# Kernel tuning notes

Hardware: AMD Instinct MI355X
Metric: run time of the kernel (lower is better)

The kernel has to match this reference:

```python
import jax, jax.numpy as jnp
import numpy as np
from jax import lax

EPS = 1e-5
KH = KW = 3
K = KH * KW


def conv3x3(x, w, b=None):
    # x: [B,Cin,H,W], w: [Cout,Cin,3,3], padding=1, stride=1
    y = lax.conv_general_dilated(x, w, (1, 1), [(1, 1), (1, 1)],
                                 dimension_numbers=("NCHW", "OIHW", "NCHW"))
    if b is not None:
        y = y + b[None, :, None, None]
    return y


def deform_conv2d(x, offset, mask, weight):
    # torchvision-style deform_conv2d v2: kernel 3x3, stride 1, pad 1, dilation 1,
    # groups=1, offset_groups=1. offset: [B,2K,H,W] (dy,dx per tap), mask: [B,K,H,W].
    B, C, H, W = x.shape
    off = offset.reshape(B, K, 2, H, W)
    kidx = jnp.arange(K)
    kdy = (kidx // KW - 1).astype(x.dtype)[None, :, None, None]  # [1,K,1,1]
    kdx = (kidx % KW - 1).astype(x.dtype)[None, :, None, None]
    yy = jnp.arange(H, dtype=x.dtype)[None, None, :, None]
    xx = jnp.arange(W, dtype=x.dtype)[None, None, None, :]
    py = yy + kdy + off[:, :, 0]  # [B,K,H,W] sampling rows
    px = xx + kdx + off[:, :, 1]  # [B,K,H,W] sampling cols

    y0 = jnp.floor(py).astype(jnp.int32)
    x0 = jnp.floor(px).astype(jnp.int32)
    wy = py - y0.astype(x.dtype)
    wx = px - x0.astype(x.dtype)

    def gather_b(xb, yc, xc):
        # xb: [C,H,W]; yc, xc: [K,H,W] -> [C,K,H,W], zeros outside image
        valid = (yc >= 0) & (yc < H) & (xc >= 0) & (xc < W)
        v = xb[:, jnp.clip(yc, 0, H - 1), jnp.clip(xc, 0, W - 1)]
        return v * valid[None].astype(xb.dtype)

    gather = jax.vmap(gather_b, in_axes=(0, 0, 0))  # over batch

    w00 = ((1 - wy) * (1 - wx))[:, None]  # [B,1,K,H,W]
    w01 = ((1 - wy) * wx)[:, None]
    w10 = (wy * (1 - wx))[:, None]
    w11 = (wy * wx)[:, None]

    sampled = (gather(x, y0, x0) * w00 + gather(x, y0, x0 + 1) * w01 +
               gather(x, y0 + 1, x0) * w10 + gather(x, y0 + 1, x0 + 1) * w11)
    sampled = sampled * mask[:, None]  # [B,C,K,H,W]
    wk = weight.reshape(weight.shape[0], weight.shape[1], K)
    return jnp.einsum("bckhw,ock->bohw", sampled, wk)


def reference(f1_feat, f3_feat, offset_w, offset_b, main_w, gamma, beta):
    concat = jnp.concatenate([f1_feat, f3_feat], axis=1)
    om = conv3x3(concat, offset_w, offset_b)  # [B,27,H,W]
    offset = om[:, :18]
    mask = jax.nn.sigmoid(om[:, 18:])
    aligned = deform_conv2d(f1_feat, offset, mask, main_w)
    # BatchNorm2d, training mode (batch statistics, biased variance)
    mean = aligned.mean(axis=(0, 2, 3))
    var = aligned.var(axis=(0, 2, 3))
    xn = (aligned - mean[None, :, None, None]) * lax.rsqrt(var + EPS)[None, :, None, None]
    return xn * gamma[None, :, None, None] + beta[None, :, None, None]


def setup_inputs() -> dict:
    key = jax.random.key(0)
    ks = jax.random.split(key, 5)
    B, C, H, W = 4, 64, 128, 128
    f1 = jax.random.normal(ks[0], (B, C, H, W), jnp.float32)
    f3 = jax.random.normal(ks[1], (B, C, H, W), jnp.float32)
    # small offset-conv init so predicted offsets stay in-image (like trained nets)
    offset_w = jax.random.normal(ks[2], (27, 2 * C, 3, 3), jnp.float32) * 0.01
    offset_b = jnp.zeros((27,), jnp.float32)
    main_w = jax.random.normal(ks[3], (C, C, 3, 3), jnp.float32) * (1.0 / np.sqrt(C * 9))
    gamma = jnp.ones((C,), jnp.float32)
    beta = jnp.zeros((C,), jnp.float32)
    return {"f1_feat": f1, "f3_feat": f3, "offset_w": offset_w,
            "offset_b": offset_b, "main_w": main_w, "gamma": gamma, "beta": beta}
```

## Files before the change

### kernel.cpp

```cpp
#include <hip/hip_runtime.h>
#include <math.h>

#define BB 4
#define CC 64
#define HH 128
#define WW 128
#define HWP 16384

typedef _Float16 h2 __attribute__((ext_vector_type(2)));
typedef _Float16 h4 __attribute__((ext_vector_type(4)));
typedef __fp16  p2 __attribute__((ext_vector_type(2)));
typedef float f32x4 __attribute__((ext_vector_type(4)));
union HU { unsigned u; h2 h; p2 p; };
union U2H { uint2 u; h4 h; };
static __device__ __forceinline__ h2 u2h(unsigned x){ HU v; v.u = x; return v.h; }
static __device__ __forceinline__ unsigned h2u(h2 x){ HU v; v.h = x; return v.u; }
static __device__ __forceinline__ unsigned pk2u(float a, float b){
    HU v; v.p = __builtin_amdgcn_cvt_pkrtz(a, b); return v.u;
}

__global__ __launch_bounds__(256) void kTm(
    const float* __restrict__ f1, const float* __restrict__ f3,
    const float* __restrict__ ow, const float* __restrict__ mw,
    unsigned* __restrict__ f13t, unsigned* __restrict__ wmf,
    unsigned* __restrict__ wof)
{
    __shared__ float lt[64*129];
    int t = threadIdx.x;
    if (blockIdx.x < 512) {
        int b = blockIdx.x >> 7, y = blockIdx.x & 127;
        unsigned* dst = f13t + ((size_t)((b << 14) + (y << 7)))*64;
        for (int half = 0; half < 2; ++half) {
            const float* src = (half == 0 ? f1 : f3) + (((size_t)b*64) << 14) + (y << 7);
#pragma unroll 4
            for (int i = 0; i < 32; ++i) {
                int idx = i*256 + t; int c = idx >> 7, x = idx & 127;
                lt[c*129 + x] = src[(c << 14) + x];
            }
            __syncthreads();
#pragma unroll 4
            for (int i = 0; i < 16; ++i) {
                int idx = i*256 + t; int x = idx >> 5, cp = idx & 31;
                dst[x*64 + half*32 + cp] = pk2u(lt[(2*cp)*129 + x], lt[(2*cp+1)*129 + x]);
            }
            __syncthreads();
        }
        return;
    }
    int i = (blockIdx.x - 512)*256 + t;
    if (i < 18432) {
        int j   = i & 1;
        int t2  = i >> 1;
        int kb  = t2 % 36;
        int rl  = t2 / 36;
        int l   = rl & 63;
        int r   = rl >> 6;
        int row = l & 15, ksel = l >> 4;
        int och = r*16 + row;
        int P   = kb*8 + ksel*2 + j;
        int kt  = P >> 5;
        int cp  = P & 31;
        float lo = mw[och*576 + (2*cp    )*9 + kt];
        float hi = mw[och*576 + (2*cp + 1)*9 + kt];
        wmf[i] = pk2u(lo, hi);
    } else if (i < 36864) {
        int idx = i - 18432;
        int j   = idx & 1;
        int t2  = idx >> 1;
        int kb  = t2 % 72;
        int rl  = t2 / 72;
        int l   = rl & 63;
        int mt  = rl >> 6;
        int row = l & 15, ksel = l >> 4;
        int och = mt*16 + row;
        int P   = kb*8 + ksel*2 + j;
        int kt  = P >> 6;
        int cp  = P & 63;
        unsigned v = 0;
        if (och < 27) {
            float lo = ow[(och*128 + 2*cp    )*9 + kt];
            float hi = ow[(och*128 + 2*cp + 1)*9 + kt];
            v = pk2u(lo, hi);
        }
        wof[idx] = v;
    }
}

__global__ __launch_bounds__(256) void k1_offset_conv(
    const unsigned* __restrict__ f13t, const unsigned* __restrict__ wof,
    const float* __restrict__ ob, float* __restrict__ om)
{
    __shared__ unsigned tile[34*68];

    int blk0 = blockIdx.x;
    int blk  = ((blk0 & 7) << 8) | (blk0 >> 3);
    int xq = blk & 3;
    int y  = (blk >> 2) & 127;
    int b  = blk >> 9;

    int tid  = threadIdx.x;
    int lane = tid & 63;
    int wv   = tid >> 6;
    int mt   = wv >> 1;
    int pxt  = wv & 1;
    int row  = lane & 15;
    int ksel = lane >> 4;

    f32x4 acc = {0.f, 0.f, 0.f, 0.f};
    const unsigned* wbase = wof + (size_t)(mt*64 + lane)*144;

#pragma unroll 1
    for (int dy = 0; dy < 3; ++dy) {
        int yy = y + dy - 1;
        bool yok = (unsigned)yy < (unsigned)HH;
        __syncthreads();
        for (int i = tid; i < 544; i += 256) {
            int px34 = i >> 4, q = i & 15;
            int gxp = xq*32 - 1 + px34;
            uint4 v = make_uint4(0u, 0u, 0u, 0u);
            if (yok && (unsigned)gxp < (unsigned)WW)
                v = *(const uint4*)&f13t[(((size_t)(b*128 + yy))*128 + gxp)*64 + q*4];
            *(uint4*)&tile[px34*68 + q*4] = v;
        }
        __syncthreads();

#pragma unroll
        for (int hf = 0; hf < 2; ++hf) {
            uint4 wq[6];
#pragma unroll
            for (int m = 0; m < 6; ++m)
                wq[m] = *(const uint4*)&wbase[dy*48 + hf*24 + m*4];
#pragma unroll
            for (int kl = 0; kl < 12; ++kl) {
                int Pl  = (hf*12 + kl)*8 + ksel*2;
                int ktl = Pl >> 6;
                int cp  = Pl & 63;
                U2H wa;
                uint4 q = wq[kl >> 1];
                if (kl & 1) { wa.u.x = q.z; wa.u.y = q.w; }
                else        { wa.u.x = q.x; wa.u.y = q.y; }
                U2H bfr;
                bfr.u = *(const uint2*)&tile[(pxt*16 + row + ktl)*68 + cp];
                acc = __builtin_amdgcn_mfma_f32_16x16x16f16(wa.h, bfr.h, acc, 0, 0, 0);
            }
        }
    }

    int gx = xq*32 + pxt*16 + row;
#pragma unroll
    for (int rI = 0; rI < 4; ++rI) {
        int och = mt*16 + ksel*4 + rI;
        if (och < 27) {
            float v = acc[rI] + ob[och];
            if (och >= 18) v = 1.f / (1.f + __expf(-v));
            om[((b*27 + och) << 14) + (y << 7) + gx] = v;
        }
    }
}

__global__ __launch_bounds__(256) void k2_deform(
    const unsigned* __restrict__ f13t, const unsigned* __restrict__ wmf,
    const float* __restrict__ om, unsigned* __restrict__ alignedh,
    float* __restrict__ part)
{
    extern __shared__ unsigned lds[];
    unsigned* pl_a = lds;
    unsigned* pl_w = lds + 288;
    unsigned* sl   = lds + 864;

    int blk0 = blockIdx.x;
    int blk  = ((blk0 & 7) << 8) | (blk0 >> 3);
    int xq = blk & 3;
    int y  = (blk >> 2) & 127;
    int b  = blk >> 9;

    int tid  = threadIdx.x;
    int lane = tid & 63;
    int wv   = tid >> 6;
    int row  = lane & 15;
    int ksel = lane >> 4;
    int cg   = tid & 7;
    int grp  = tid >> 3;
    int pwb  = ((cg >> 2) << 4) | ((cg & 1) << 3) | (((cg >> 1) & 1) << 1);

    const float* omb = om + ((b*27) << 14) + (y << 7);
    const unsigned* ftb = f13t + (((size_t)b) << 20);

    for (int i = tid; i < 288; i += 256) {
        int k = i >> 5, lpx = i & 31;
        int gxp = xq*32 + lpx;
        float off0 = omb[((2*k)   << 14) + gxp];
        float off1 = omb[((2*k+1) << 14) + gxp];
        float mk   = omb[((18+k)  << 14) + gxp];

        float pyf = (float)y   + (float)(k/3) - 1.f + off0;
        float pxg = (float)gxp + (float)(k%3) - 1.f + off1;
        float fy = floorf(pyf), fx = floorf(pxg);
        int y0 = (int)fy, x0 = (int)fx;
        float wy = pyf - fy, wx = pxg - fx;
        float oy = 1.f - wy, ox = 1.f - wx;
        bool yv0 = (unsigned)y0     < (unsigned)HH;
        bool yv1 = (unsigned)(y0+1) < (unsigned)HH;
        bool xv0 = (unsigned)x0     < (unsigned)WW;
        bool xv1 = (unsigned)(x0+1) < (unsigned)WW;
        int y0c = min(max(y0, 0), 127);
        int x0c = min(max(x0, 0), 127);
        int dy = min(max(y0+1, 0), 127) - y0c;
        int dx = min(max(x0+1, 0), 127) - x0c;
        unsigned a = (unsigned)((y0c << 7) + x0c) | ((unsigned)dx << 14) | ((unsigned)dy << 15);
        float w00 = (yv0 && xv0) ? oy*ox*mk : 0.f;
        float w01 = (yv0 && xv1) ? oy*wx*mk : 0.f;
        float w10 = (yv1 && xv0) ? wy*ox*mk : 0.f;
        float w11 = (yv1 && xv1) ? wy*wx*mk : 0.f;
        pl_a[i] = a;
        pl_w[i*2]     = pk2u(w00, w01);
        pl_w[i*2 + 1] = pk2u(w10, w11);
    }
    __syncthreads();

    f32x4 acc0 = {0.f, 0.f, 0.f, 0.f};
    f32x4 acc1 = {0.f, 0.f, 0.f, 0.f};

    const unsigned* wbase = wmf + (wv*64 + lane)*72;

#pragma unroll 1
    for (int th = 0; th < 3; ++th) {
        uint4 wq[6];
#pragma unroll
        for (int m = 0; m < 6; ++m)
            wq[m] = *(const uint4*)&wbase[th*24 + m*4];

#pragma unroll
        for (int it = 0; it < 3; ++it) {
            int item = it*32 + grp;
            int ktl  = item >> 5;
            int px   = item & 31;
            int k    = th*3 + ktl;
            int pidx = k*32 + px;
            unsigned a = pl_a[pidx];
            uint2 wpk = *(const uint2*)&pl_w[pidx*2];
            int i00 = (int)(a & 0x3FFFu);
            int dx  = (int)((a >> 14) & 1u);
            int i10 = i00 + (((int)(a >> 15) & 1) << 7);
            h2 hw01 = u2h(wpk.x);
            h2 hw23 = u2h(wpk.y);
            h2 w00d = {hw01.x, hw01.x}, w01d = {hw01.y, hw01.y};
            h2 w10d = {hw23.x, hw23.x}, w11d = {hw23.y, hw23.y};

            uint4 t00 = *(const uint4*)&ftb[(size_t)(i00     )*64 + 4*cg];
            uint4 t01 = *(const uint4*)&ftb[(size_t)(i00 + dx)*64 + 4*cg];
            uint4 t10 = *(const uint4*)&ftb[(size_t)(i10     )*64 + 4*cg];
            uint4 t11 = *(const uint4*)&ftb[(size_t)(i10 + dx)*64 + 4*cg];

            h2 v0 = u2h(t00.x)*w00d + u2h(t01.x)*w01d + u2h(t10.x)*w10d + u2h(t11.x)*w11d;
            h2 v1 = u2h(t00.y)*w00d + u2h(t01.y)*w01d + u2h(t10.y)*w10d + u2h(t11.y)*w11d;
            h2 v2 = u2h(t00.z)*w00d + u2h(t01.z)*w01d + u2h(t10.z)*w10d + u2h(t11.z)*w11d;
            h2 v3 = u2h(t00.w)*w00d + u2h(t01.w)*w01d + u2h(t10.w)*w10d + u2h(t11.w)*w11d;

            int bs = px*100 + ktl*32 + pwb;
            *(uint2*)&sl[bs]     = make_uint2(h2u(v0), h2u(v1));
            *(uint2*)&sl[bs + 4] = make_uint2(h2u(v2), h2u(v3));
        }
        __syncthreads();

        const unsigned* b0p = &sl[(row     )*100 + ksel*4];
        const unsigned* b1p = &sl[(16+row  )*100 + ksel*4];
#pragma unroll
        for (int m = 0; m < 6; ++m) {
            uint4 bv0 = *(const uint4*)&b0p[m*16];
            uint4 bv1 = *(const uint4*)&b1p[m*16];
            U2H waA, waB, s0a, s0b, s1a, s1b;
            waA.u.x = wq[m].x; waA.u.y = wq[m].y;
            waB.u.x = wq[m].z; waB.u.y = wq[m].w;
            s0a.u.x = bv0.x; s0a.u.y = bv0.y;
            s0b.u.x = bv0.z; s0b.u.y = bv0.w;
            s1a.u.x = bv1.x; s1a.u.y = bv1.y;
            s1b.u.x = bv1.z; s1b.u.y = bv1.w;
            acc0 = __builtin_amdgcn_mfma_f32_16x16x16f16(waA.h, s0a.h, acc0, 0, 0, 0);
            acc0 = __builtin_amdgcn_mfma_f32_16x16x16f16(waB.h, s0b.h, acc0, 0, 0, 0);
            acc1 = __builtin_amdgcn_mfma_f32_16x16x16f16(waA.h, s1a.h, acc1, 0, 0, 0);
            acc1 = __builtin_amdgcn_mfma_f32_16x16x16f16(waB.h, s1b.h, acc1, 0, 0, 0);
        }
        __syncthreads();
    }

    float* sred = (float*)lds;
    int obase = ((b*CC) << 13) + (y << 6) + (xq << 4);
#pragma unroll
    for (int rI = 0; rI < 4; ++rI) {
        int och = wv*16 + ksel*4 + rI;
        float v0 = acc0[rI], v1 = acc1[rI];
        alignedh[obase + (och << 13) + row] = pk2u(v0, v1);
        float s  = v0 + v1;
        float sq = v0*v0 + v1*v1;
#pragma unroll
        for (int off = 1; off < 16; off <<= 1) {
            s  += __shfl_xor(s,  off, 64);
            sq += __shfl_xor(sq, off, 64);
        }
        if (row == 0) { sred[och] = s; sred[64 + och] = sq; }
    }
    __syncthreads();
    for (int i = tid; i < 128; i += 256)
        part[(size_t)blk*128 + i] = sred[i];
}

__global__ __launch_bounds__(256) void k3b_reduce(
    const float* __restrict__ part, float* __restrict__ stats)
{
    int i = blockIdx.x;
    int tid = threadIdx.x;
    float s = 0.f;
    for (int j = tid; j < 2048; j += 256) s += part[(size_t)j*128 + i];
    for (int off = 32; off > 0; off >>= 1) s += __shfl_down(s, off, 64);
    __shared__ float rs[4];
    int w = tid >> 6;
    if ((tid & 63) == 0) rs[w] = s;
    __syncthreads();
    if (tid == 0) stats[i] = rs[0] + rs[1] + rs[2] + rs[3];
}

__global__ __launch_bounds__(256) void k4_norm(
    const unsigned* __restrict__ alignedh, const float* __restrict__ stats,
    const float* __restrict__ gamma, const float* __restrict__ beta,
    float* __restrict__ out)
{
    const float invN = 1.f / 65536.f;
    int i4 = blockIdx.x*256 + threadIdx.x;
    int u  = i4 << 2;
    int c  = (u >> 13) & 63;
    int lx = u & 15;
    int xq = (u >> 4) & 3;
    int y  = (u >> 6) & 127;
    int bc = u >> 13;

    float mean = stats[c] * invN;
    float var  = stats[64 + c] * invN - mean*mean;
    float sc = gamma[c] * rsqrtf(var + 1e-5f);
    float sh = beta[c] - mean*sc;

    uint4 v = *(const uint4*)&alignedh[u];
    h2 p0 = u2h(v.x), p1 = u2h(v.y), p2 = u2h(v.z), p3 = u2h(v.w);
    float4 lo = make_float4((float)p0.x*sc + sh, (float)p1.x*sc + sh,
                            (float)p2.x*sc + sh, (float)p3.x*sc + sh);
    float4 hi = make_float4((float)p0.y*sc + sh, (float)p1.y*sc + sh,
                            (float)p2.y*sc + sh, (float)p3.y*sc + sh);
    int ob = (bc << 14) + (y << 7) + xq*32 + lx;
    *(float4*)&out[ob]      = lo;
    *(float4*)&out[ob + 16] = hi;
}

extern "C" void kernel_launch(void* const* d_in, const int* in_sizes, int n_in,
                              void* d_out, int out_size, void* d_ws, size_t ws_size,
                              hipStream_t stream)
{
    const float* f1    = (const float*)d_in[0];
    const float* f3    = (const float*)d_in[1];
    const float* ow    = (const float*)d_in[2];
    const float* ob    = (const float*)d_in[3];
    const float* mw    = (const float*)d_in[4];
    const float* gamma = (const float*)d_in[5];
    const float* beta  = (const float*)d_in[6];
    float* out = (float*)d_out;

    float* om     = (float*)d_ws;
    float* stats  = om + 4*27*HWP;
    unsigned* wmf = (unsigned*)(stats + 512);
    unsigned* wof = wmf + 18432;
    unsigned* f13t = wof + 18432;
    float* part   = (float*)(f13t + 4*HWP*64);
    unsigned* alignedh = (unsigned*)(part + 2048*128);

    const int lds2 = (864 + 32*100) * 4;
    (void)hipFuncSetAttribute((const void*)k2_deform,
        hipFuncAttributeMaxDynamicSharedMemorySize, lds2);

    hipLaunchKernelGGL(kTm, dim3(656), dim3(256), 0, stream,
                       f1, f3, ow, mw, f13t, wmf, wof);
    hipLaunchKernelGGL(k1_offset_conv, dim3(2048), dim3(256), 0, stream,
                       f13t, wof, ob, om);
    hipLaunchKernelGGL(k2_deform, dim3(2048), dim3(256), lds2, stream,
                       f13t, wmf, om, alignedh, part);
    hipLaunchKernelGGL(k3b_reduce, dim3(128), dim3(256), 0, stream, part, stats);
    hipLaunchKernelGGL(k4_norm, dim3(2048), dim3(256), 0, stream,
                       alignedh, stats, gamma, beta, out);
}
```

Before: 78.38 us.

## Compute two output rows per block in offset conv, reusing halo rows and weights

The offset-conv kernel now handles two output rows per block instead of one. It loads all four needed input rows into a larger dynamic LDS buffer with a single barrier, and each wave computes 32 pixels using two accumulators that share each weight fragment. This cuts redundant halo-row loads, weight fetches from global memory and barriers, and halves the grid to 1024 blocks. In exchange, LDS per block grows to about 37KB, which may lower occupancy, and the reduced grid leaves less parallelism.

```diff
diff --git a/kernel.cpp b/kernel.cpp
--- a/kernel.cpp
+++ b/kernel.cpp
@@ -90,40 +90,46 @@
     const unsigned* __restrict__ f13t, const unsigned* __restrict__ wof,
     const float* __restrict__ ob, float* __restrict__ om)
 {
-    __shared__ unsigned tile[34*68];
+    extern __shared__ unsigned tile[];
 
     int blk0 = blockIdx.x;
-    int blk  = ((blk0 & 7) << 8) | (blk0 >> 3);
+    int blk  = ((blk0 & 7) << 7) | (blk0 >> 3);
     int xq = blk & 3;
-    int y  = (blk >> 2) & 127;
-    int b  = blk >> 9;
+    int yp = (blk >> 2) & 63;
+    int b  = blk >> 8;
+    int y0r = yp << 1;
 
     int tid  = threadIdx.x;
     int lane = tid & 63;
     int wv   = tid >> 6;
     int mt   = wv >> 1;
-    int pxt  = wv & 1;
+    int ys   = wv & 1;
     int row  = lane & 15;
     int ksel = lane >> 4;
 
-    f32x4 acc = {0.f, 0.f, 0.f, 0.f};
-    const unsigned* wbase = wof + (size_t)(mt*64 + lane)*144;
-
 #pragma unroll 1
-    for (int dy = 0; dy < 3; ++dy) {
-        int yy = y + dy - 1;
+    for (int s = 0; s < 4; ++s) {
+        int yy = y0r + s - 1;
         bool yok = (unsigned)yy < (unsigned)HH;
-        __syncthreads();
+        unsigned* ts = tile + s*2312;
         for (int i = tid; i < 544; i += 256) {
             int px34 = i >> 4, q = i & 15;
             int gxp = xq*32 - 1 + px34;
             uint4 v = make_uint4(0u, 0u, 0u, 0u);
             if (yok && (unsigned)gxp < (unsigned)WW)
                 v = *(const uint4*)&f13t[(((size_t)(b*128 + yy))*128 + gxp)*64 + q*4];
-            *(uint4*)&tile[px34*68 + q*4] = v;
-        }
-        __syncthreads();
-
+            *(uint4*)&ts[px34*68 + q*4] = v;
+        }
+    }
+    __syncthreads();
+
+    f32x4 acc0 = {0.f, 0.f, 0.f, 0.f};
+    f32x4 acc1 = {0.f, 0.f, 0.f, 0.f};
+    const unsigned* wbase = wof + (size_t)(mt*64 + lane)*144;
+
+#pragma unroll 1
+    for (int dy = 0; dy < 3; ++dy) {
+        const unsigned* ts = tile + (ys + dy)*2312;
 #pragma unroll
         for (int hf = 0; hf < 2; ++hf) {
             uint4 wq[6];
@@ -139,21 +145,30 @@
                 uint4 q = wq[kl >> 1];
                 if (kl & 1) { wa.u.x = q.z; wa.u.y = q.w; }
                 else        { wa.u.x = q.x; wa.u.y = q.y; }
-                U2H bfr;
-                bfr.u = *(const uint2*)&tile[(pxt*16 + row + ktl)*68 + cp];
-                acc = __builtin_amdgcn_mfma_f32_16x16x16f16(wa.h, bfr.h, acc, 0, 0, 0);
+                U2H b0, b1;
+                b0.u = *(const uint2*)&ts[(row + ktl)*68 + cp];
+                b1.u = *(const uint2*)&ts[(16 + row + ktl)*68 + cp];
+                acc0 = __builtin_amdgcn_mfma_f32_16x16x16f16(wa.h, b0.h, acc0, 0, 0, 0);
+                acc1 = __builtin_amdgcn_mfma_f32_16x16x16f16(wa.h, b1.h, acc1, 0, 0, 0);
             }
         }
     }
 
-    int gx = xq*32 + pxt*16 + row;
+    int y  = y0r + ys;
+    int gx0 = xq*32 + row;
 #pragma unroll
     for (int rI = 0; rI < 4; ++rI) {
         int och = mt*16 + ksel*4 + rI;
         if (och < 27) {
-            float v = acc[rI] + ob[och];
-            if (och >= 18) v = 1.f / (1.f + __expf(-v));
-            om[((b*27 + och) << 14) + (y << 7) + gx] = v;
+            float v0 = acc0[rI] + ob[och];
+            float v1 = acc1[rI] + ob[och];
+            if (och >= 18) {
+                v0 = 1.f / (1.f + __expf(-v0));
+                v1 = 1.f / (1.f + __expf(-v1));
+            }
+            int base = ((b*27 + och) << 14) + (y << 7) + gx0;
+            om[base]      = v0;
+            om[base + 16] = v1;
         }
     }
 }
@@ -371,13 +386,16 @@
     float* part   = (float*)(f13t + 4*HWP*64);
     unsigned* alignedh = (unsigned*)(part + 2048*128);
 
+    const int lds1 = 4*2312*4;
     const int lds2 = (864 + 32*100) * 4;
+    (void)hipFuncSetAttribute((const void*)k1_offset_conv,
+        hipFuncAttributeMaxDynamicSharedMemorySize, lds1);
     (void)hipFuncSetAttribute((const void*)k2_deform,
         hipFuncAttributeMaxDynamicSharedMemorySize, lds2);
 
     hipLaunchKernelGGL(kTm, dim3(656), dim3(256), 0, stream,
                        f1, f3, ow, mw, f13t, wmf, wof);
-    hipLaunchKernelGGL(k1_offset_conv, dim3(2048), dim3(256), 0, stream,
+    hipLaunchKernelGGL(k1_offset_conv, dim3(1024), dim3(256), lds1, stream,
                        f13t, wof, ob, om);
     hipLaunchKernelGGL(k2_deform, dim3(2048), dim3(256), lds2, stream,
                        f13t, wmf, om, alignedh, part);
```

Result: faster. 69.99 us (-10.7%).
